# Kernel optimization log

Hardware: AMD Instinct MI355X
Metric: run time of the kernel (lower is better)

## Reference

```python
import jax, jax.numpy as jnp
import numpy as np

NEG_SLOPE = 0.2  # PyG RGATConv default negative_slope


def _rgat_conv(x, src, dst, edge_type, W, q, k, b, num_nodes):
    # W: [R, in, H] per-relation weight (heads=1 so H = heads*out_channels)
    # Transform every node by every relation once, then gather per edge
    # (same math as PyG's per-edge bmm with index_select'd weights, but
    #  avoids materializing [E, in, H] weights).
    xr = jnp.einsum('ni,rio->rno', x, W)            # [R, N, H]
    qv = jnp.einsum('rno,oh->rnh', xr, q)           # [R, N, heads]
    kv = jnp.einsum('rno,oh->rnh', xr, k)           # [R, N, heads]
    # additive self-attention: alpha_e = leaky_relu(q(out_i) + k(out_j))
    alpha = qv[edge_type, dst] + kv[edge_type, src]  # [E, heads]
    alpha = jnp.where(alpha >= 0, alpha, NEG_SLOPE * alpha)
    # softmax over incoming edges of each destination node (across-relation)
    amax = jax.ops.segment_max(alpha, dst, num_segments=num_nodes)  # [N, heads]
    amax = jnp.where(jnp.isfinite(amax), amax, 0.0)
    ex = jnp.exp(alpha - amax[dst])
    denom = jax.ops.segment_sum(ex, dst, num_segments=num_nodes)
    att = ex / (denom[dst] + 1e-16)                 # [E, heads]
    msg = xr[edge_type, src] * att                  # [E, H] (heads=1 broadcast)
    out = jax.ops.segment_sum(msg, dst, num_segments=num_nodes)    # [N, H]
    return out + b


def setup_inputs() -> dict:
    key = jax.random.key(0)
    ks = jax.random.split(key, 16)
    N, E, R, IN, H = 50000, 800000, 8, 128, 128
    x = jax.random.normal(ks[0], (N, IN), dtype=jnp.float32)
    edge_index = jax.random.randint(ks[1], (2, E), 0, N, dtype=jnp.int32)
    edge_type = jax.random.randint(ks[2], (E,), 0, R, dtype=jnp.int32)
    s_in = 1.0 / np.sqrt(IN)
    s_h = 1.0 / np.sqrt(H)
    w0 = jax.random.normal(ks[3], (R, IN, H), dtype=jnp.float32) * s_in
    q0 = jax.random.normal(ks[4], (H, 1), dtype=jnp.float32) * s_h
    k0 = jax.random.normal(ks[5], (H, 1), dtype=jnp.float32) * s_h
    b0 = jnp.zeros((H,), dtype=jnp.float32)
    w1 = jax.random.normal(ks[6], (R, H, H), dtype=jnp.float32) * s_h
    q1 = jax.random.normal(ks[7], (H, 1), dtype=jnp.float32) * s_h
    k1 = jax.random.normal(ks[8], (H, 1), dtype=jnp.float32) * s_h
    b1 = jnp.zeros((H,), dtype=jnp.float32)
    fc1_w = jax.random.normal(ks[9], (2 * H, H), dtype=jnp.float32) * (1.0 / np.sqrt(2 * H))
    fc1_b = jnp.zeros((H,), dtype=jnp.float32)
    fc2_w = jax.random.normal(ks[10], (H, 1), dtype=jnp.float32) * s_h
    fc2_b = jnp.zeros((1,), dtype=jnp.float32)
    return {"x": x, "edge_index": edge_index, "edge_type": edge_type,
            "w0": w0, "q0": q0, "k0": k0, "b0": b0,
            "w1": w1, "q1": q1, "k1": k1, "b1": b1,
            "fc1_w": fc1_w, "fc1_b": fc1_b, "fc2_w": fc2_w, "fc2_b": fc2_b}


def reference(x, edge_index, edge_type, w0, q0, k0, b0, w1, q1, k1, b1, fc1_w, fc1_b, fc2_w, fc2_b):
    N = x.shape[0]
    src, dst = edge_index[0], edge_index[1]
    h = jax.nn.relu(_rgat_conv(x, src, dst, edge_type, w0, q0, k0, b0, N))
    h = jax.nn.relu(_rgat_conv(h, src, dst, edge_type, w1, q1, k1, b1, N))
    g = jnp.concatenate([h.mean(axis=0), h.max(axis=0)], axis=-1)  # [2H]
    g = jnp.tanh(g)
    g = jax.nn.relu(g @ fc1_w + fc1_b)   # dropout is identity in eval mode
    out = g @ fc2_w + fc2_b              # [1]
    return jax.nn.sigmoid(out)
```

## Files before the change

### kernel.cpp

```cpp
#include <hip/hip_runtime.h>
#include <hip/hip_bf16.h>


typedef __bf16 bf16x8 __attribute__((ext_vector_type(8)));
typedef __bf16 bf16x4 __attribute__((ext_vector_type(4)));
typedef __bf16 bf16x2 __attribute__((ext_vector_type(2)));
typedef float f32x4 __attribute__((ext_vector_type(4)));

#define CBSH 10
#define CSC_CH 4096


__global__ __launch_bounds__(256) void k_chist(const int* __restrict__ dst, int* __restrict__ chist, int E) {
  __shared__ int lh[64];
  int t = threadIdx.x;
  if (t < 64) lh[t] = 0;
  __syncthreads();
  for (int e = blockIdx.x * 256 + t; e < E; e += gridDim.x * 256)
    atomicAdd(&lh[dst[e] >> CBSH], 1);
  __syncthreads();
  if (t < 64 && lh[t]) atomicAdd(&chist[t], lh[t]);
}

__global__ __launch_bounds__(256) void k_cscatter(const int* __restrict__ src, const int* __restrict__ dst,
                                                  const int* __restrict__ et, const int* __restrict__ chist,
                                                  int* __restrict__ ccur0, int* __restrict__ tmp, int E) {
  __shared__ int recbuf[CSC_CH];
  __shared__ int lcnt[64], lbase[64], gbase[64], lcur[64], cb[64];
  int t = threadIdx.x;
  int base = blockIdx.x * CSC_CH;
  int cnt = E - base; if (cnt > CSC_CH) cnt = CSC_CH;
  if (t < 64) { lcnt[t] = 0; cb[t] = chist[t]; }
  __syncthreads();
  int myrec[CSC_CH / 256], mycb[CSC_CH / 256];
  int k = 0;
  for (int i = t; i < cnt; i += 256, ++k) {
    int d = dst[base + i];
    int c = d >> CBSH;
    myrec[k] = src[base + i] | (et[base + i] << 17) | ((d & ((1 << CBSH) - 1)) << 20);
    mycb[k] = c;
    atomicAdd(&lcnt[c], 1);
  }
  __syncthreads();
  if (t == 0) {
    int acc = 0, acc2 = 0;
    for (int c = 0; c < 64; ++c) {
      lbase[c] = acc; lcur[c] = acc; acc += lcnt[c];
      int h = cb[c]; cb[c] = acc2; acc2 += h;
    }
  }
  __syncthreads();
  if (t < 64 && lcnt[t] > 0) gbase[t] = cb[t] + atomicAdd(&ccur0[t], lcnt[t]);
  __syncthreads();
  k = 0;
  for (int i = t; i < cnt; i += 256, ++k) {
    int p = atomicAdd(&lcur[mycb[k]], 1);
    recbuf[p] = myrec[k];
  }
  __syncthreads();
  for (int i = t; i < cnt; i += 256) {
    int lo = 0, hi = 63;
    while (lo < hi) { int mid = (lo + hi + 1) >> 1; if (lbase[mid] <= i) lo = mid; else hi = mid - 1; }
    tmp[gbase[lo] + (i - lbase[lo])] = recbuf[i];
  }
}

__global__ __launch_bounds__(1024) void k_fsort(const int* __restrict__ chist, const int* __restrict__ tmp,
                                                int* __restrict__ recs, int* __restrict__ row_ptr,
                                                int N, int E) {
  __shared__ int sd[1024];
  __shared__ int ncur[1024];
  __shared__ int cbs[65];
  int cb = blockIdx.x, t = threadIdx.x;
  int n0 = cb << CBSH;
  if (t < 64) cbs[t] = chist[t];
  __syncthreads();
  if (t == 0) {
    int acc = 0;
    for (int c = 0; c < 64; ++c) { int h = cbs[c]; cbs[c] = acc; acc += h; }
    cbs[64] = acc;
  }
  sd[t] = 0;
  __syncthreads();
  int begin = cbs[cb], endd = cbs[cb + 1];
  for (int i = begin + t; i < endd; i += 1024)
    atomicAdd(&sd[(tmp[i] >> 20) & 1023], 1);
  __syncthreads();
  int myc = sd[t];
  for (int off = 1; off < 1024; off <<= 1) {
    int xv = 0; if (t >= off) xv = sd[t - off];
    __syncthreads();
    sd[t] += xv;
    __syncthreads();
  }
  int ex = sd[t] - myc;
  int node = n0 + t;
  if (node < N) row_ptr[node] = begin + ex;
  if (node == N - 1) row_ptr[N] = E;
  ncur[t] = begin + ex;
  __syncthreads();
  for (int i = begin + t; i < endd; i += 1024) {
    int rc = tmp[i];
    int p = atomicAdd(&ncur[(rc >> 20) & 1023], 1);
    recs[p] = rc & 0xFFFFF;
  }
}


__global__ __launch_bounds__(256) void k_wprep(const float* __restrict__ W, const float* __restrict__ q,
                                               const float* __restrict__ k, __bf16* __restrict__ wqkb,
                                               __bf16* __restrict__ WT) {
  if (blockIdx.x < 256) {
    int g = blockIdx.x * 4 + (threadIdx.x >> 6);
    int lane = threadIdx.x & 63;
    const float2* wrow = (const float2*)(W + (size_t)g * 128);
    float2 wv = wrow[lane];
    float2 qv2 = ((const float2*)q)[lane];
    float2 kv2 = ((const float2*)k)[lane];
    float aq = wv.x * qv2.x + wv.y * qv2.y;
    float ak = wv.x * kv2.x + wv.y * kv2.y;
    #pragma unroll
    for (int off = 32; off; off >>= 1) {
      aq += __shfl_xor(aq, off, 64);
      ak += __shfl_xor(ak, off, 64);
    }
    if (lane == 0) { wqkb[g] = (__bf16)aq; wqkb[1024 + g] = (__bf16)ak; }
  } else {
    __shared__ float t[32][33];
    int bb = blockIdx.x - 256;
    int r = bb >> 4;
    int rem = bb & 15;
    int k0 = (rem & 3) * 32, h0 = (rem >> 2) * 32;
    int tx = threadIdx.x & 31;
    int ty = threadIdx.x >> 5;
    #pragma unroll
    for (int i = 0; i < 4; ++i) {
      int kk = ty + i * 8;
      t[kk][tx] = W[((size_t)r * 128 + k0 + kk) * 128 + h0 + tx];
    }
    __syncthreads();
    #pragma unroll
    for (int i = 0; i < 4; ++i) {
      int hh = ty + i * 8;
      WT[(size_t)(h0 + hh) * 1024 + r * 128 + k0 + tx] = (__bf16)t[tx][hh];
    }
  }
}


#define ASTR 136

template <int L0>
__global__ __launch_bounds__(256) void k_gemmY(const void* __restrict__ xin,
                                               const __bf16* __restrict__ WT2,
                                               const __bf16* __restrict__ wqkb,
                                               __bf16* __restrict__ Y, float* __restrict__ qkv, int M) {
  __shared__ __bf16 As[128 * ASTR];
  __shared__ __bf16 Bs[128 * ASTR];
  int bm = blockIdx.x * 128;
  int tid = threadIdx.x;
  int w = tid >> 6, l = tid & 63;
  int srow = tid >> 1;
  int cb8 = (tid & 1) * 8;
  bool valid = (bm + srow) < M;

  if (L0) {
    const float* gA = (const float*)xin + (size_t)(bm + srow) * 128 + cb8 * 8;
    #pragma unroll
    for (int i = 0; i < 8; ++i) {
      float4 f0 = make_float4(0.f, 0.f, 0.f, 0.f), f1 = f0;
      if (valid) { f0 = *(const float4*)(gA + i * 8); f1 = *(const float4*)(gA + i * 8 + 4); }
      bf16x8 v;
      v[0] = (__bf16)f0.x; v[1] = (__bf16)f0.y; v[2] = (__bf16)f0.z; v[3] = (__bf16)f0.w;
      v[4] = (__bf16)f1.x; v[5] = (__bf16)f1.y; v[6] = (__bf16)f1.z; v[7] = (__bf16)f1.w;
      *(bf16x8*)&As[srow * ASTR + (cb8 + i) * 8] = v;
    }
  } else {
    const bf16x8* gA = (const bf16x8*)((const __bf16*)xin + (size_t)(bm + srow) * 128);
    #pragma unroll
    for (int i = 0; i < 8; ++i) {
      bf16x8 v = valid ? gA[cb8 + i] : (bf16x8)(__bf16)0.0f;
      *(bf16x8*)&As[srow * ASTR + (cb8 + i) * 8] = v;
    }
  }
  {
    int qr = tid >> 4, qc = tid & 15;
    *(bf16x8*)&Bs[qr * ASTR + qc * 8] = *(const bf16x8*)(wqkb + (size_t)qr * 128 + qc * 8);
  }
  __syncthreads();

  {
    f32x4 qacc[2];
    qacc[0] = (f32x4)0.f; qacc[1] = (f32x4)0.f;
    #pragma unroll
    for (int ks = 0; ks < 4; ++ks) {
      bf16x8 bq = *(const bf16x8*)&Bs[(l & 15) * ASTR + ks * 32 + (l >> 4) * 8];
      #pragma unroll
      for (int m2 = 0; m2 < 2; ++m2) {
        bf16x8 af = *(const bf16x8*)&As[(w * 32 + m2 * 16 + (l & 15)) * ASTR + ks * 32 + (l >> 4) * 8];
        qacc[m2] = __builtin_amdgcn_mfma_f32_16x16x32_bf16(af, bq, qacc[m2], 0, 0, 0);
      }
    }
    #pragma unroll
    for (int m2 = 0; m2 < 2; ++m2)
      #pragma unroll
      for (int j = 0; j < 4; ++j) {
        int row = w * 32 + m2 * 16 + (l >> 4) * 4 + j;
        if (bm + row < M) qkv[(size_t)(bm + row) * 16 + (l & 15)] = qacc[m2][j];
      }
  }

  for (int r = 0; r < 8; ++r) {
    __syncthreads();
    {
      const bf16x8* gB = (const bf16x8*)(WT2 + (size_t)srow * 1024 + r * 128);
      #pragma unroll
      for (int i = 0; i < 8; ++i)
        *(bf16x8*)&Bs[srow * ASTR + (cb8 + i) * 8] = gB[cb8 + i];
    }
    __syncthreads();

    f32x4 acc[2][8];
    #pragma unroll
    for (int m2 = 0; m2 < 2; ++m2)
      #pragma unroll
      for (int n2 = 0; n2 < 8; ++n2) acc[m2][n2] = (f32x4)0.f;

    #pragma unroll
    for (int ks = 0; ks < 4; ++ks) {
      bf16x8 af[2], bfv[8];
      #pragma unroll
      for (int m2 = 0; m2 < 2; ++m2)
        af[m2] = *(const bf16x8*)&As[(w * 32 + m2 * 16 + (l & 15)) * ASTR + ks * 32 + (l >> 4) * 8];
      #pragma unroll
      for (int n2 = 0; n2 < 8; ++n2)
        bfv[n2] = *(const bf16x8*)&Bs[(n2 * 16 + (l & 15)) * ASTR + ks * 32 + (l >> 4) * 8];
      #pragma unroll
      for (int m2 = 0; m2 < 2; ++m2)
        #pragma unroll
        for (int n2 = 0; n2 < 8; ++n2)
          acc[m2][n2] = __builtin_amdgcn_mfma_f32_16x16x32_bf16(af[m2], bfv[n2], acc[m2][n2], 0, 0, 0);
    }

    __bf16* Yr = Y + ((size_t)r * M + bm) * 128;
    #pragma unroll
    for (int m2 = 0; m2 < 2; ++m2)
      #pragma unroll
      for (int j = 0; j < 4; ++j) {
        int row = w * 32 + m2 * 16 + (l >> 4) * 4 + j;
        if (bm + row < M) {
          #pragma unroll
          for (int n2 = 0; n2 < 8; ++n2)
            Yr[(size_t)row * 128 + n2 * 16 + (l & 15)] = (__bf16)acc[m2][n2][j];
        }
      }
  }
}


__global__ __launch_bounds__(256) void k_aggY(const int* __restrict__ row_ptr, const int* __restrict__ recs,
                                              const float* __restrict__ qkv, const __bf16* __restrict__ Y,
                                              const float* __restrict__ bias, __bf16* __restrict__ hout,
                                              int N) {
  int wv = threadIdx.x >> 6;
  int lane = threadIdx.x & 63;
  int n = blockIdx.x * 4 + wv;
  if (n >= N) return;
  int start = row_ptr[n], end = row_ptr[n + 1];
  const float* qvn = qkv + (size_t)n * 16;
  float denom = 0.f, m_run = -1e30f;
  int sub = lane & 15;
  int grp = lane >> 4;
  float acc[8];
  #pragma unroll
  for (int j = 0; j < 8; ++j) acc[j] = 0.f;

  for (int c0 = start; c0 < end; c0 += 64) {
    int cend = (end < c0 + 64) ? end : (c0 + 64);
    int cnt = cend - c0;
    int p = c0 + lane;
    float a = -1e30f; int rec = 0;
    if (p < cend) {
      rec = recs[p];
      int s = rec & 0x1FFFF, r = (rec >> 17) & 7;
      float t = qvn[r] + qkv[(size_t)s * 16 + 8 + r];
      a = (t >= 0.f) ? t : 0.2f * t;
    }
    float cm = a;
    #pragma unroll
    for (int off = 32; off; off >>= 1) cm = fmaxf(cm, __shfl_xor(cm, off, 64));
    if (cm > m_run) {
      if (m_run > -1e29f) {
        float scale = __expf(m_run - cm);
        denom *= scale;
        #pragma unroll
        for (int j = 0; j < 8; ++j) acc[j] *= scale;
      }
      m_run = cm;
    }
    float wgt = (p < cend) ? __expf(a - m_run) : 0.f;
    float ws = wgt;
    #pragma unroll
    for (int off = 32; off; off >>= 1) ws += __shfl_xor(ws, off, 64);
    denom += ws;
    int wbits = __float_as_int(wgt);

    int nbatch = (cnt + 3) >> 2;
    #pragma unroll 2
    for (int b = 0; b < nbatch; ++b) {
      int idx = grp * 4 + b * 16;
      int rg = __builtin_amdgcn_ds_bpermute(idx, rec);
      int wg = __builtin_amdgcn_ds_bpermute(idx, wbits);
      float fw = __int_as_float(wg);
      int s_ = rg & 0x1FFFF;
      int r_ = (rg >> 17) & 7;
      bf16x8 xv = *(const bf16x8*)(Y + ((size_t)r_ * N + s_) * 128 + sub * 8);
      #pragma unroll
      for (int j = 0; j < 8; ++j) acc[j] += fw * (float)xv[j];
    }
  }

  #pragma unroll
  for (int j = 0; j < 8; ++j) {
    acc[j] += __shfl_xor(acc[j], 16, 64);
    acc[j] += __shfl_xor(acc[j], 32, 64);
  }
  float inv = 1.f / (denom + 1e-16f);
  if (grp == 0) {
    float4 b0 = *(const float4*)(bias + sub * 8);
    float4 b1 = *(const float4*)(bias + sub * 8 + 4);
    float bb[8] = {b0.x, b0.y, b0.z, b0.w, b1.x, b1.y, b1.z, b1.w};
    bf16x8 o;
    #pragma unroll
    for (int j = 0; j < 8; ++j) o[j] = (__bf16)fmaxf(acc[j] * inv + bb[j], 0.f);
    *(bf16x8*)(hout + (size_t)n * 128 + sub * 8) = o;
  }
}


__global__ __launch_bounds__(256) void k_pool(const __bf16* __restrict__ h, float* __restrict__ gsum,
                                              float* __restrict__ gmax, int N) {
  int c2 = threadIdx.x & 63;
  int grp = threadIdx.x >> 6;
  float s0 = 0.f, s1 = 0.f, m0 = 0.f, m1 = 0.f;
  for (int n = blockIdx.x * 4 + grp; n < N; n += gridDim.x * 4) {
    bf16x2 v = ((const bf16x2*)(h + (size_t)n * 128))[c2];
    float v0 = (float)v.x, v1 = (float)v.y;
    s0 += v0; s1 += v1;
    m0 = fmaxf(m0, v0); m1 = fmaxf(m1, v1);
  }
  __shared__ float ss0[256], ss1[256], sm0[256], sm1[256];
  ss0[threadIdx.x] = s0; ss1[threadIdx.x] = s1;
  sm0[threadIdx.x] = m0; sm1[threadIdx.x] = m1;
  __syncthreads();
  if (grp == 0) {
    #pragma unroll
    for (int g = 1; g < 4; ++g) {
      s0 += ss0[g * 64 + c2]; s1 += ss1[g * 64 + c2];
      m0 = fmaxf(m0, sm0[g * 64 + c2]); m1 = fmaxf(m1, sm1[g * 64 + c2]);
    }
    atomicAdd(&gsum[2 * c2 + 0], s0);
    atomicAdd(&gsum[2 * c2 + 1], s1);
    atomicMax((int*)gmax + 2 * c2 + 0, __float_as_int(m0));
    atomicMax((int*)gmax + 2 * c2 + 1, __float_as_int(m1));
  }
}

__global__ void k_head(const float* __restrict__ gsum, const float* __restrict__ gmax,
                       const float* __restrict__ fc1w, const float* __restrict__ fc1b,
                       const float* __restrict__ fc2w, const float* __restrict__ fc2b,
                       float* __restrict__ out, int N) {
  __shared__ float g[256];
  __shared__ float red[128];
  int t = threadIdx.x;
  if (t < 128) g[t] = tanhf(gsum[t] / (float)N);
  else g[t] = tanhf(gmax[t - 128]);
  __syncthreads();
  float r1 = 0.f;
  if (t < 128) {
    float a = fc1b[t];
    for (int i = 0; i < 256; i++) a += g[i] * fc1w[i * 128 + t];
    r1 = a > 0.f ? a : 0.f;
    red[t] = r1 * fc2w[t];
  }
  __syncthreads();
  for (int s = 64; s > 0; s >>= 1) {
    if (t < s) red[t] += red[t + s];
    __syncthreads();
  }
  if (t == 0) {
    float o = red[0] + fc2b[0];
    out[0] = 1.f / (1.f + __expf(-o));
  }
}


extern "C" void kernel_launch(void* const* d_in, const int* in_sizes, int n_in,
                              void* d_out, int out_size, void* d_ws, size_t ws_size,
                              hipStream_t stream) {
  const float* x    = (const float*)d_in[0];
  const int*   ei   = (const int*)d_in[1];
  const int*   ety  = (const int*)d_in[2];
  const float* w0   = (const float*)d_in[3];
  const float* q0   = (const float*)d_in[4];
  const float* k0   = (const float*)d_in[5];
  const float* b0   = (const float*)d_in[6];
  const float* w1   = (const float*)d_in[7];
  const float* q1   = (const float*)d_in[8];
  const float* k1   = (const float*)d_in[9];
  const float* b1   = (const float*)d_in[10];
  const float* fc1w = (const float*)d_in[11];
  const float* fc1b = (const float*)d_in[12];
  const float* fc2w = (const float*)d_in[13];
  const float* fc2b = (const float*)d_in[14];
  int N = in_sizes[0] / 128;
  int E = in_sizes[2];
  const int* src = ei;
  const int* dst = ei + E;

  char* base = (char*)d_ws;
  size_t off = 0;
  auto alloc = [&](size_t bytes) -> void* {
    off = (off + 255) & ~(size_t)255;
    void* p = base + off;
    off += bytes;
    return p;
  };
  int ncb = (N + (1 << CBSH) - 1) >> CBSH;

  int*    row_ptr = (int*)alloc((size_t)(N + 1) * 4);
  int*    csrctr  = (int*)alloc(128 * 4);
  int*    chist   = csrctr;
  int*    ccur0   = csrctr + 64;
  int*    tmp     = (int*)alloc((size_t)E * 4);
  int*    recs    = (int*)alloc((size_t)E * 4);
  float*  qkv     = (float*)alloc((size_t)N * 16 * 4);
  float*  gpool   = (float*)alloc(256 * 4);
  float*  gsum    = gpool;
  float*  gmax    = gpool + 128;
  __bf16* wqkb    = (__bf16*)alloc(2048 * 2);
  __bf16* h1b     = (__bf16*)alloc((size_t)N * 128 * 2);
  __bf16* h2b     = (__bf16*)alloc((size_t)N * 128 * 2);
  __bf16* WT2     = (__bf16*)alloc((size_t)128 * 1024 * 2);
  __bf16* Y       = (__bf16*)alloc((size_t)8 * N * 128 * 2);

  hipMemsetAsync(csrctr, 0, 128 * 4, stream);
  k_chist<<<256, 256, 0, stream>>>(dst, chist, E);
  k_cscatter<<<(E + CSC_CH - 1) / CSC_CH, 256, 0, stream>>>(src, dst, ety, chist, ccur0, tmp, E);
  k_fsort<<<ncb, 1024, 0, stream>>>(chist, tmp, recs, row_ptr, N, E);

  for (int layer = 0; layer < 2; ++layer) {
    const float*  W    = layer ? w1 : w0;
    const float*  qq   = layer ? q1 : q0;
    const float*  kk   = layer ? k1 : k0;
    const float*  bb   = layer ? b1 : b0;
    __bf16*       hout = layer ? h2b : h1b;

    k_wprep<<<384, 256, 0, stream>>>(W, qq, kk, wqkb, WT2);
    if (layer == 0)
      k_gemmY<1><<<(N + 127) / 128, 256, 0, stream>>>((const void*)x, WT2, wqkb, Y, qkv, N);
    else
      k_gemmY<0><<<(N + 127) / 128, 256, 0, stream>>>((const void*)h1b, WT2, wqkb, Y, qkv, N);
    k_aggY<<<(N + 3) / 4, 256, 0, stream>>>(row_ptr, recs, qkv, Y, bb, hout, N);
  }

  hipMemsetAsync(gpool, 0, 256 * 4, stream);
  k_pool<<<256, 256, 0, stream>>>(h2b, gsum, gmax, N);
  k_head<<<1, 256, 0, stream>>>(gsum, gmax, fc1w, fc1b, fc2w, fc2b, (float*)d_out, N);
}
```

Baseline: 258.6 us.

## Store per-relation transformed features as FP8 and batch both layers' weight prep

The per-relation node transforms Y are now stored as FP8 (e4m3) instead of bf16. This halves the bytes the edge-aggregation kernel gathers per edge and the bytes the GEMM writes. Both layers' weight preparation now runs in one launch at the start, and the two control memsets are merged into one. The cost is a large drop in precision for the gathered messages, which may push the output past tolerance.

```diff
diff --git a/kernel.cpp b/kernel.cpp
--- a/kernel.cpp
+++ b/kernel.cpp
@@ -6,6 +6,7 @@
 typedef __bf16 bf16x4 __attribute__((ext_vector_type(4)));
 typedef __bf16 bf16x2 __attribute__((ext_vector_type(2)));
 typedef float f32x4 __attribute__((ext_vector_type(4)));
+typedef float f32x2 __attribute__((ext_vector_type(2)));
 
 #define CBSH 10
 #define CSC_CH 4096
@@ -107,11 +108,20 @@
 }
 
 
-__global__ __launch_bounds__(256) void k_wprep(const float* __restrict__ W, const float* __restrict__ q,
-                                               const float* __restrict__ k, __bf16* __restrict__ wqkb,
-                                               __bf16* __restrict__ WT) {
-  if (blockIdx.x < 256) {
-    int g = blockIdx.x * 4 + (threadIdx.x >> 6);
+__global__ __launch_bounds__(256) void k_wprep(const float* __restrict__ w0, const float* __restrict__ q0,
+                                               const float* __restrict__ k0, const float* __restrict__ w1,
+                                               const float* __restrict__ q1, const float* __restrict__ k1,
+                                               __bf16* __restrict__ wqkb, __bf16* __restrict__ WT) {
+  int layer = blockIdx.x >> 9;
+  int bx = blockIdx.x;
+  if (bx >= 384) { layer = 1; bx -= 384; } else layer = 0;
+  const float* W = layer ? w1 : w0;
+  const float* q = layer ? q1 : q0;
+  const float* k = layer ? k1 : k0;
+  __bf16* wq = wqkb + layer * 2048;
+  __bf16* WTl = WT + (size_t)layer * 131072;
+  if (bx < 256) {
+    int g = bx * 4 + (threadIdx.x >> 6);
     int lane = threadIdx.x & 63;
     const float2* wrow = (const float2*)(W + (size_t)g * 128);
     float2 wv = wrow[lane];
@@ -124,25 +134,25 @@
       aq += __shfl_xor(aq, off, 64);
       ak += __shfl_xor(ak, off, 64);
     }
-    if (lane == 0) { wqkb[g] = (__bf16)aq; wqkb[1024 + g] = (__bf16)ak; }
+    if (lane == 0) { wq[g] = (__bf16)aq; wq[1024 + g] = (__bf16)ak; }
   } else {
     __shared__ float t[32][33];
-    int bb = blockIdx.x - 256;
+    int bb = bx - 256;
     int r = bb >> 4;
     int rem = bb & 15;
-    int k0 = (rem & 3) * 32, h0 = (rem >> 2) * 32;
+    int kk0 = (rem & 3) * 32, h0 = (rem >> 2) * 32;
     int tx = threadIdx.x & 31;
     int ty = threadIdx.x >> 5;
     #pragma unroll
     for (int i = 0; i < 4; ++i) {
       int kk = ty + i * 8;
-      t[kk][tx] = W[((size_t)r * 128 + k0 + kk) * 128 + h0 + tx];
+      t[kk][tx] = W[((size_t)r * 128 + kk0 + kk) * 128 + h0 + tx];
     }
     __syncthreads();
     #pragma unroll
     for (int i = 0; i < 4; ++i) {
       int hh = ty + i * 8;
-      WT[(size_t)(h0 + hh) * 1024 + r * 128 + k0 + tx] = (__bf16)t[tx][hh];
+      WTl[(size_t)(h0 + hh) * 1024 + r * 128 + kk0 + tx] = (__bf16)t[tx][hh];
     }
   }
 }
@@ -154,7 +164,7 @@
 __global__ __launch_bounds__(256) void k_gemmY(const void* __restrict__ xin,
                                                const __bf16* __restrict__ WT2,
                                                const __bf16* __restrict__ wqkb,
-                                               __bf16* __restrict__ Y, float* __restrict__ qkv, int M) {
+                                               unsigned char* __restrict__ Y, float* __restrict__ qkv, int M) {
   __shared__ __bf16 As[128 * ASTR];
   __shared__ __bf16 Bs[128 * ASTR];
   int bm = blockIdx.x * 128;
@@ -242,7 +252,7 @@
           acc[m2][n2] = __builtin_amdgcn_mfma_f32_16x16x32_bf16(af[m2], bfv[n2], acc[m2][n2], 0, 0, 0);
     }
 
-    __bf16* Yr = Y + ((size_t)r * M + bm) * 128;
+    unsigned char* Yr = Y + ((size_t)r * M + bm) * 128;
     #pragma unroll
     for (int m2 = 0; m2 < 2; ++m2)
       #pragma unroll
@@ -250,8 +260,11 @@
         int row = w * 32 + m2 * 16 + (l >> 4) * 4 + j;
         if (bm + row < M) {
           #pragma unroll
-          for (int n2 = 0; n2 < 8; ++n2)
-            Yr[(size_t)row * 128 + n2 * 16 + (l & 15)] = (__bf16)acc[m2][n2][j];
+          for (int n2 = 0; n2 < 8; ++n2) {
+            float v = acc[m2][n2][j];
+            int pk = __builtin_amdgcn_cvt_pk_fp8_f32(v, v, 0, false);
+            Yr[(size_t)row * 128 + n2 * 16 + (l & 15)] = (unsigned char)(pk & 0xFF);
+          }
         }
       }
   }
@@ -259,7 +272,7 @@
 
 
 __global__ __launch_bounds__(256) void k_aggY(const int* __restrict__ row_ptr, const int* __restrict__ recs,
-                                              const float* __restrict__ qkv, const __bf16* __restrict__ Y,
+                                              const float* __restrict__ qkv, const unsigned char* __restrict__ Y,
                                               const float* __restrict__ bias, __bf16* __restrict__ hout,
                                               int N) {
   int wv = threadIdx.x >> 6;
@@ -314,9 +327,15 @@
       float fw = __int_as_float(wg);
       int s_ = rg & 0x1FFFF;
       int r_ = (rg >> 17) & 7;
-      bf16x8 xv = *(const bf16x8*)(Y + ((size_t)r_ * N + s_) * 128 + sub * 8);
-      #pragma unroll
-      for (int j = 0; j < 8; ++j) acc[j] += fw * (float)xv[j];
+      int2 xv = *(const int2*)(Y + (((size_t)r_ * N + s_) << 7) + sub * 8);
+      f32x2 f01 = __builtin_amdgcn_cvt_pk_f32_fp8(xv.x, false);
+      f32x2 f23 = __builtin_amdgcn_cvt_pk_f32_fp8(xv.x, true);
+      f32x2 f45 = __builtin_amdgcn_cvt_pk_f32_fp8(xv.y, false);
+      f32x2 f67 = __builtin_amdgcn_cvt_pk_f32_fp8(xv.y, true);
+      acc[0] += fw * f01[0]; acc[1] += fw * f01[1];
+      acc[2] += fw * f23[0]; acc[3] += fw * f23[1];
+      acc[4] += fw * f45[0]; acc[5] += fw * f45[1];
+      acc[6] += fw * f67[0]; acc[7] += fw * f67[1];
     }
   }
 
@@ -429,42 +448,38 @@
   int ncb = (N + (1 << CBSH) - 1) >> CBSH;
 
   int*    row_ptr = (int*)alloc((size_t)(N + 1) * 4);
-  int*    csrctr  = (int*)alloc(128 * 4);
-  int*    chist   = csrctr;
-  int*    ccur0   = csrctr + 64;
+  int*    ctrl    = (int*)alloc(384 * 4);
+  int*    chist   = ctrl;
+  int*    ccur0   = ctrl + 64;
+  float*  gpool   = (float*)(ctrl + 128);
+  float*  gsum    = gpool;
+  float*  gmax    = gpool + 128;
   int*    tmp     = (int*)alloc((size_t)E * 4);
   int*    recs    = (int*)alloc((size_t)E * 4);
   float*  qkv     = (float*)alloc((size_t)N * 16 * 4);
-  float*  gpool   = (float*)alloc(256 * 4);
-  float*  gsum    = gpool;
-  float*  gmax    = gpool + 128;
-  __bf16* wqkb    = (__bf16*)alloc(2048 * 2);
+  __bf16* wqkb    = (__bf16*)alloc(2 * 2048 * 2);
   __bf16* h1b     = (__bf16*)alloc((size_t)N * 128 * 2);
   __bf16* h2b     = (__bf16*)alloc((size_t)N * 128 * 2);
-  __bf16* WT2     = (__bf16*)alloc((size_t)128 * 1024 * 2);
-  __bf16* Y       = (__bf16*)alloc((size_t)8 * N * 128 * 2);
-
-  hipMemsetAsync(csrctr, 0, 128 * 4, stream);
+  __bf16* WT2     = (__bf16*)alloc((size_t)2 * 131072 * 2);
+  unsigned char* Y = (unsigned char*)alloc((size_t)8 * N * 128);
+
+  hipMemsetAsync(ctrl, 0, 384 * 4, stream);
   k_chist<<<256, 256, 0, stream>>>(dst, chist, E);
   k_cscatter<<<(E + CSC_CH - 1) / CSC_CH, 256, 0, stream>>>(src, dst, ety, chist, ccur0, tmp, E);
   k_fsort<<<ncb, 1024, 0, stream>>>(chist, tmp, recs, row_ptr, N, E);
 
+  k_wprep<<<768, 256, 0, stream>>>(w0, q0, k0, w1, q1, k1, wqkb, WT2);
+
   for (int layer = 0; layer < 2; ++layer) {
-    const float*  W    = layer ? w1 : w0;
-    const float*  qq   = layer ? q1 : q0;
-    const float*  kk   = layer ? k1 : k0;
-    const float*  bb   = layer ? b1 : b0;
-    __bf16*       hout = layer ? h2b : h1b;
-
-    k_wprep<<<384, 256, 0, stream>>>(W, qq, kk, wqkb, WT2);
+    const float* bb   = layer ? b1 : b0;
+    __bf16*      hout = layer ? h2b : h1b;
     if (layer == 0)
       k_gemmY<1><<<(N + 127) / 128, 256, 0, stream>>>((const void*)x, WT2, wqkb, Y, qkv, N);
     else
-      k_gemmY<0><<<(N + 127) / 128, 256, 0, stream>>>((const void*)h1b, WT2, wqkb, Y, qkv, N);
+      k_gemmY<0><<<(N + 127) / 128, 256, 0, stream>>>((const void*)h1b, WT2 + 131072, wqkb + 2048, Y, qkv, N);
     k_aggY<<<(N + 3) / 4, 256, 0, stream>>>(row_ptr, recs, qkv, Y, bb, hout, N);
   }
 
-  hipMemsetAsync(gpool, 0, 256 * 4, stream);
   k_pool<<<256, 256, 0, stream>>>(h2b, gsum, gmax, N);
   k_head<<<1, 256, 0, stream>>>(gsum, gmax, fc1w, fc1b, fc2w, fc2b, (float*)d_out, N);
 }
```

Measured after the change: 242.3 us. -6.3%, faster.
